# Optimization experiments

Hardware: AMD Instinct MI355X
Metric: run time of the kernel (lower is better)

Reference implementation:

```python
import jax, jax.numpy as jnp
import numpy as np

D_MODEL = 1024
N_HEADS = 16
D_HEAD = D_MODEL // N_HEADS
D_FF = 4096
B, T = 4, 2048
LN_EPS = 1e-5


def _layer_norm(x, gamma, beta):
    mu = jnp.mean(x, axis=-1, keepdims=True)
    var = jnp.var(x, axis=-1, keepdims=True)
    return (x - mu) * jax.lax.rsqrt(var + LN_EPS) * gamma + beta


def setup_inputs() -> dict:
    key = jax.random.key(0)
    ks = jax.random.split(key, 8)
    x = jax.random.normal(ks[0], (B, T, D_MODEL), dtype=jnp.float32)
    # causal mask: True = blocked (upper triangle above diagonal)
    attn_mask = ~jnp.tril(jnp.ones((T, T), dtype=bool))
    # xavier-uniform linear weights stored as [in, out] (pytorch applies x @ W.T)
    def xavier(k, fan_in, fan_out):
        lim = float(np.sqrt(6.0 / (fan_in + fan_out)))
        return jax.random.uniform(k, (fan_in, fan_out), jnp.float32, -lim, lim)
    Wq = xavier(ks[1], D_MODEL, D_MODEL); bq = jnp.zeros((D_MODEL,), jnp.float32)
    Wk = xavier(ks[2], D_MODEL, D_MODEL); bk = jnp.zeros((D_MODEL,), jnp.float32)
    Wv = xavier(ks[3], D_MODEL, D_MODEL); bv = jnp.zeros((D_MODEL,), jnp.float32)
    Wo = xavier(ks[4], D_MODEL, D_MODEL); bo = jnp.zeros((D_MODEL,), jnp.float32)
    W1 = xavier(ks[5], D_MODEL, D_FF); b1 = jnp.zeros((D_FF,), jnp.float32)
    W2 = 0.02 * jax.random.normal(ks[6], (D_FF, D_MODEL), jnp.float32)  # normal std=0.02 per _init_weights
    b2 = jnp.zeros((D_MODEL,), jnp.float32)
    g1 = jnp.ones((D_MODEL,), jnp.float32); be1 = jnp.zeros((D_MODEL,), jnp.float32)
    g2 = jnp.ones((D_MODEL,), jnp.float32); be2 = jnp.zeros((D_MODEL,), jnp.float32)
    return {"x": x, "attn_mask": attn_mask,
            "Wq": Wq, "bq": bq, "Wk": Wk, "bk": bk, "Wv": Wv, "bv": bv,
            "Wo": Wo, "bo": bo, "W1": W1, "b1": b1, "W2": W2, "b2": b2,
            "g1": g1, "be1": be1, "g2": g2, "be2": be2}


def reference(x, attn_mask, Wq, bq, Wk, bk, Wv, bv, Wo, bo, W1, b1, W2, b2, g1, be1, g2, be2):
    Bd, Td, Dd = x.shape
    residual = x
    x_n = _layer_norm(x, g1, be1)
    # projections -> (B, H, T, Dh)
    q = (x_n @ Wq + bq).reshape(Bd, Td, N_HEADS, D_HEAD).transpose(0, 2, 1, 3)
    k = (x_n @ Wk + bk).reshape(Bd, Td, N_HEADS, D_HEAD).transpose(0, 2, 1, 3)
    v = (x_n @ Wv + bv).reshape(Bd, Td, N_HEADS, D_HEAD).transpose(0, 2, 1, 3)
    scale = 1.0 / jnp.sqrt(jnp.asarray(D_HEAD, x.dtype))
    scores = jnp.einsum('bhqd,bhkd->bhqk', q, k) * scale  # (B,H,T,T)
    scores = jnp.where(attn_mask[None, None], -jnp.inf, scores)
    attn = jax.nn.softmax(scores, axis=-1)
    attn_out = jnp.einsum('bhqk,bhkd->bhqd', attn, v)
    attn_out = attn_out.transpose(0, 2, 1, 3).reshape(Bd, Td, Dd)
    attn_out = attn_out @ Wo + bo
    x = residual + attn_out  # dropout = identity (p=0 / eval)
    h = _layer_norm(x, g2, be2)
    h = jax.nn.gelu(h @ W1 + b1, approximate=False) @ W2 + b2
    return x + h
```

## Files before the change

kernel.cpp:

```cpp
#include <hip/hip_runtime.h>
#include <hip/hip_bf16.h>
#include <math.h>

#define TT   2048
#define DD   1024
#define HHD  16
#define FFD  4096
#define NTOK 8192

typedef __attribute__((ext_vector_type(8))) short bf16x8;
typedef __attribute__((ext_vector_type(4))) float f32x4;
typedef unsigned int u32;
#define AS(n) __attribute__((address_space(n)))

__device__ __forceinline__ unsigned short f2bf(float f) {
    u32 u = __builtin_bit_cast(u32, f);
    u += 0x7fffu + ((u >> 16) & 1u);
    return (unsigned short)(u >> 16);
}

__device__ __forceinline__ void gld_lds16(const void* g, void* l) {
    __builtin_amdgcn_global_load_lds((const AS(1) u32*)g, (AS(3) u32*)l, 16, 0, 0);
}

__device__ __forceinline__ int swz(int row) { return (row + (row >> 3)) & 7; }

__global__ __launch_bounds__(256) void wtrans(const float* __restrict__ W,
                                              unsigned short* __restrict__ Wt,
                                              int K, int N) {
    __shared__ float t[32][33];
    int tx = threadIdx.x & 31, ty = threadIdx.x >> 5;
    int n0 = blockIdx.x * 32, k0 = blockIdx.y * 32;
    #pragma unroll
    for (int i = 0; i < 32; i += 8)
        t[ty + i][tx] = W[(size_t)(k0 + ty + i) * N + n0 + tx];
    __syncthreads();
    #pragma unroll
    for (int i = 0; i < 32; i += 8)
        Wt[(size_t)(n0 + ty + i) * K + k0 + tx] = f2bf(t[tx][ty + i]);
}

__global__ __launch_bounds__(256) void ln_bf16(const float* __restrict__ x,
                                               const float* __restrict__ g,
                                               const float* __restrict__ be,
                                               unsigned short* __restrict__ y) {
    int tok = blockIdx.x, tid = threadIdx.x;
    float4 v = ((const float4*)(x + (size_t)tok * DD))[tid];
    float s  = v.x + v.y + v.z + v.w;
    float ss = v.x*v.x + v.y*v.y + v.z*v.z + v.w*v.w;
    #pragma unroll
    for (int m = 32; m >= 1; m >>= 1) { s += __shfl_xor(s, m); ss += __shfl_xor(ss, m); }
    __shared__ float red[8];
    if ((tid & 63) == 0) { red[tid >> 6] = s; red[4 + (tid >> 6)] = ss; }
    __syncthreads();
    s  = red[0] + red[1] + red[2] + red[3];
    ss = red[4] + red[5] + red[6] + red[7];
    float mu   = s * (1.0f / DD);
    float rstd = rsqrtf(ss * (1.0f / DD) - mu * mu + 1e-5f);
    float4 gv = ((const float4*)g)[tid];
    float4 bv = ((const float4*)be)[tid];
    ushort4 o;
    o.x = f2bf((v.x - mu) * rstd * gv.x + bv.x);
    o.y = f2bf((v.y - mu) * rstd * gv.y + bv.y);
    o.z = f2bf((v.z - mu) * rstd * gv.z + bv.z);
    o.w = f2bf((v.w - mu) * rstd * gv.w + bv.w);
    *(ushort4*)(y + (size_t)tok * DD + tid * 4) = o;
}

template <int MODE>
__global__ __launch_bounds__(256, 3) void gemm_bf16(const unsigned short* __restrict__ A,
                                                    const unsigned short* __restrict__ Bt,
                                                    const float* __restrict__ bias,
                                                    void* __restrict__ C,
                                                    const float* __restrict__ resid,
                                                    int M, int N, int K) {
    __shared__ __align__(16) unsigned short As[128 * 64];
    __shared__ __align__(16) unsigned short Bs[128 * 64];
    int tid = threadIdx.x, lane = tid & 63, w = tid >> 6;
    int wm = w >> 1, wn = w & 1;
    int m0 = blockIdx.y * 128, n0 = blockIdx.x * 128;
    int c = lane & 15, g = lane >> 4;

    f32x4 acc[4][4];
    f32x4 z4 = {0.f, 0.f, 0.f, 0.f};
    #pragma unroll
    for (int i = 0; i < 4; ++i)
        #pragma unroll
        for (int j = 0; j < 4; ++j) acc[i][j] = z4;

    const unsigned short* aSrc[4];
    const unsigned short* bSrc[4];
    int ldsOff[4];
    #pragma unroll
    for (int i = 0; i < 4; ++i) {
        int inst = w * 4 + i;
        int row  = inst * 8 + (lane >> 3);
        int kk   = ((lane & 7) ^ swz(row)) << 3;
        aSrc[i] = A  + (size_t)(m0 + row) * K + kk;
        bSrc[i] = Bt + (size_t)(n0 + row) * K + kk;
        ldsOff[i] = inst * 1024;
    }

    for (int k0 = 0; k0 < K; k0 += 64) {
        #pragma unroll
        for (int i = 0; i < 4; ++i) {
            gld_lds16(aSrc[i] + k0, (char*)As + ldsOff[i]);
            gld_lds16(bSrc[i] + k0, (char*)Bs + ldsOff[i]);
        }
        __syncthreads();
        #pragma unroll
        for (int ks = 0; ks < 2; ++ks) {
            bf16x8 af[4], bfr[4];
            int slot = ks * 4 + g;
            #pragma unroll
            for (int f = 0; f < 4; ++f) {
                int ra = wm * 64 + f * 16 + c;
                af[f]  = *(const bf16x8*)((const char*)As + ra * 128 + ((slot ^ swz(ra)) << 4));
                int rb = wn * 64 + f * 16 + c;
                bfr[f] = *(const bf16x8*)((const char*)Bs + rb * 128 + ((slot ^ swz(rb)) << 4));
            }
            #pragma unroll
            for (int i = 0; i < 4; ++i)
                #pragma unroll
                for (int j = 0; j < 4; ++j)
                    acc[i][j] = __builtin_amdgcn_mfma_f32_16x16x32_bf16(af[i], bfr[j], acc[i][j], 0, 0, 0);
        }
        __syncthreads();
    }

    float bcol[4];
    float4 brow[4];
    if (MODE == 4) {
        #pragma unroll
        for (int i = 0; i < 4; ++i)
            brow[i] = *(const float4*)&bias[m0 + wm * 64 + i * 16 + g * 4];
    } else {
        #pragma unroll
        for (int j = 0; j < 4; ++j) bcol[j] = bias[n0 + wn * 64 + j * 16 + c];
    }
    #pragma unroll
    for (int i = 0; i < 4; ++i) {
        #pragma unroll
        for (int r = 0; r < 4; ++r) {
            int rowm = m0 + wm * 64 + i * 16 + g * 4 + r;
            float br = (MODE == 4) ? ((const float*)&brow[i])[r] : 0.0f;
            #pragma unroll
            for (int j = 0; j < 4; ++j) {
                float val = acc[i][j][r] + ((MODE == 4) ? br : bcol[j]);
                int col = n0 + wn * 64 + j * 16 + c;
                if (MODE == 1) {
                    int b = rowm >> 11, t = rowm & 2047, h = col >> 6, d = col & 63;
                    ((unsigned short*)C)[(((size_t)((b << 4) + h) * TT + t) << 6) + d] = f2bf(val);
                } else if (MODE == 2) {
                    size_t idx = (size_t)rowm * N + col;
                    ((float*)C)[idx] = val + resid[idx];
                } else if (MODE == 3) {
                    float ge = 0.5f * val * (1.0f + erff(val * 0.70710678118f));
                    ((unsigned short*)C)[(size_t)rowm * N + col] = f2bf(ge);
                } else {
                    int b = col >> 11, t = col & 2047, h = rowm >> 6, d = rowm & 63;
                    ((unsigned short*)C)[(((size_t)((b << 4) + h) * 64 + d) << 11) + t] = f2bf(val);
                }
            }
        }
    }
}

__global__ __launch_bounds__(256, 4) void attn_bf16(const unsigned short* __restrict__ q,
                                                    const unsigned short* __restrict__ k,
                                                    const unsigned short* __restrict__ vt,
                                                    unsigned short* __restrict__ ao) {
    __shared__ __align__(16) unsigned short Ks[2][64 * 64];
    __shared__ __align__(16) unsigned short Vts[2][64 * 64];
    __shared__ __align__(16) unsigned short Ps[4][16 * 64];
    int tid = threadIdx.x, lane = tid & 63, w = tid >> 6;
    int bid = blockIdx.x;
    int bh  = (bid & 7) * 8 + ((bid >> 3) & 7);
    int pr  = bid >> 6;
    int c = lane & 15, g = lane >> 4;
    size_t kbase = (size_t)bh * TT * 64;
    size_t vbase = (size_t)bh * 64 * TT;

    const unsigned short* kSrc[2];
    const unsigned short* vSrc[2];
    int ldsOff[2];
    #pragma unroll
    for (int i = 0; i < 2; ++i) {
        int inst = w * 2 + i;
        int row  = inst * 8 + (lane >> 3);
        int kk   = ((lane & 7) ^ swz(row)) << 3;
        kSrc[i] = k  + kbase + (size_t)row * 64 + kk;
        vSrc[i] = vt + vbase + (size_t)row * TT + kk;
        ldsOff[i] = inst * 1024;
    }

    auto STAGE = [&](int buf, int kv0) {
        #pragma unroll
        for (int i = 0; i < 2; ++i) {
            gld_lds16(kSrc[i] + (size_t)kv0 * 64, (char*)Ks[buf] + ldsOff[i]);
            gld_lds16(vSrc[i] + kv0,              (char*)Vts[buf] + ldsOff[i]);
        }
    };

    int b = bh >> 4, h = bh & 15;
    f32x4 z4 = {0.f, 0.f, 0.f, 0.f};

    for (int ph = 0; ph < 2; ++ph) {
        int qt = ph ? (31 - pr) : pr;
        int q0 = qt * 64;
        int qrow = q0 + w * 16 + c;
        bf16x8 qf[2];
        qf[0] = *(const bf16x8*)(q + kbase + (size_t)qrow * 64 + g * 8);
        qf[1] = *(const bf16x8*)(q + kbase + (size_t)qrow * 64 + 32 + g * 8);

        float m_i[4], l_i[4];
        f32x4 o[4];
        #pragma unroll
        for (int j = 0; j < 4; ++j) { m_i[j] = -INFINITY; l_i[j] = 0.0f; o[j] = z4; }

        __syncthreads();
        STAGE(0, 0);

        for (int kt = 0; kt <= qt; ++kt) {
            int cur = kt & 1, kv0 = kt * 64;
            __syncthreads();
            if (kt < qt) STAGE(cur ^ 1, kv0 + 64);

            f32x4 s[4];
            #pragma unroll
            for (int f = 0; f < 4; ++f) s[f] = z4;
            __builtin_amdgcn_s_setprio(1);
            #pragma unroll
            for (int ks = 0; ks < 2; ++ks) {
                int slot = ks * 4 + g;
                #pragma unroll
                for (int f = 0; f < 4; ++f) {
                    int rb = f * 16 + c;
                    bf16x8 kf = *(const bf16x8*)((const char*)Ks[cur] + rb * 128 + ((slot ^ swz(rb)) << 4));
                    s[f] = __builtin_amdgcn_mfma_f32_16x16x32_bf16(qf[ks], kf, s[f], 0, 0, 0);
                }
            }
            __builtin_amdgcn_s_setprio(0);

            bool diag = (kt == qt);
            #pragma unroll
            for (int j = 0; j < 4; ++j) {
                int lq = g * 4 + j;
                int gq = q0 + w * 16 + lq;
                #pragma unroll
                for (int f = 0; f < 4; ++f) {
                    float sv = s[f][j] * 0.125f;
                    if (diag && (kv0 + f * 16 + c > gq)) sv = -INFINITY;
                    s[f][j] = sv;
                }
                float mx = fmaxf(fmaxf(s[0][j], s[1][j]), fmaxf(s[2][j], s[3][j]));
                #pragma unroll
                for (int mm = 8; mm >= 1; mm >>= 1) mx = fmaxf(mx, __shfl_xor(mx, mm));
                float newm = fmaxf(m_i[j], mx);
                float al = __expf(m_i[j] - newm);
                float rs = 0.0f;
                #pragma unroll
                for (int f = 0; f < 4; ++f) {
                    float p = __expf(s[f][j] - newm);
                    s[f][j] = p;
                    rs += p;
                }
                #pragma unroll
                for (int mm = 8; mm >= 1; mm >>= 1) rs += __shfl_xor(rs, mm);
                l_i[j] = l_i[j] * al + rs;
                m_i[j] = newm;
                #pragma unroll
                for (int f = 0; f < 4; ++f) {
                    int col = f * 16 + c;
                    int byte = lq * 128 + (((col >> 3) ^ swz(lq)) << 4) + ((col & 7) << 1);
                    *(unsigned short*)((char*)Ps[w] + byte) = f2bf(s[f][j]);
                }
                #pragma unroll
                for (int fd = 0; fd < 4; ++fd) o[fd][j] *= al;
            }
            asm volatile("s_waitcnt lgkmcnt(0)" ::: "memory");
            __builtin_amdgcn_sched_barrier(0);

            __builtin_amdgcn_s_setprio(1);
            #pragma unroll
            for (int ks = 0; ks < 2; ++ks) {
                int slot = ks * 4 + g;
                bf16x8 pa = *(const bf16x8*)((const char*)Ps[w] + c * 128 + ((slot ^ swz(c)) << 4));
                #pragma unroll
                for (int fd = 0; fd < 4; ++fd) {
                    int rv = fd * 16 + c;
                    bf16x8 vf = *(const bf16x8*)((const char*)Vts[cur] + rv * 128 + ((slot ^ swz(rv)) << 4));
                    o[fd] = __builtin_amdgcn_mfma_f32_16x16x32_bf16(pa, vf, o[fd], 0, 0, 0);
                }
            }
            __builtin_amdgcn_s_setprio(0);
        }

        #pragma unroll
        for (int fd = 0; fd < 4; ++fd)
            #pragma unroll
            for (int j = 0; j < 4; ++j) {
                int t = q0 + w * 16 + g * 4 + j;
                float val = o[fd][j] / l_i[j];
                ao[(((size_t)(b * TT + t)) << 10) + (h << 6) + fd * 16 + c] = f2bf(val);
            }
    }
}

extern "C" void kernel_launch(void* const* d_in, const int* in_sizes, int n_in,
                              void* d_out, int out_size, void* d_ws, size_t ws_size,
                              hipStream_t stream) {
    const float* x   = (const float*)d_in[0];
    const float* Wq  = (const float*)d_in[2];
    const float* bq  = (const float*)d_in[3];
    const float* Wk  = (const float*)d_in[4];
    const float* bk  = (const float*)d_in[5];
    const float* Wv  = (const float*)d_in[6];
    const float* bv  = (const float*)d_in[7];
    const float* Wo  = (const float*)d_in[8];
    const float* bo  = (const float*)d_in[9];
    const float* W1  = (const float*)d_in[10];
    const float* b1  = (const float*)d_in[11];
    const float* W2  = (const float*)d_in[12];
    const float* b2  = (const float*)d_in[13];
    const float* g1  = (const float*)d_in[14];
    const float* be1 = (const float*)d_in[15];
    const float* g2  = (const float*)d_in[16];
    const float* be2 = (const float*)d_in[17];

    float* out = (float*)d_out;
    char* w = (char*)d_ws;
    const size_t MB = 1024 * 1024;
    unsigned short* xnb = (unsigned short*)(w);
    unsigned short* qb  = (unsigned short*)(w + 16 * MB);
    unsigned short* kb  = (unsigned short*)(w + 32 * MB);
    unsigned short* vb  = (unsigned short*)(w + 48 * MB);
    unsigned short* aob = (unsigned short*)(w + 64 * MB);
    unsigned short* wqt = (unsigned short*)(w + 80 * MB);
    unsigned short* wkt = wqt + 1 * MB;
    unsigned short* wvt = wqt + 2 * MB;
    unsigned short* wot = wqt + 3 * MB;
    unsigned short* w1t = wqt + 4 * MB;
    unsigned short* w2t = w1t + 4 * MB;
    unsigned short* h1  = qb;

    dim3 blk(256);
    wtrans<<<dim3(DD / 32, DD / 32), blk, 0, stream>>>(Wq, wqt, DD, DD);
    wtrans<<<dim3(DD / 32, DD / 32), blk, 0, stream>>>(Wk, wkt, DD, DD);
    wtrans<<<dim3(DD / 32, DD / 32), blk, 0, stream>>>(Wv, wvt, DD, DD);
    wtrans<<<dim3(DD / 32, DD / 32), blk, 0, stream>>>(Wo, wot, DD, DD);
    wtrans<<<dim3(FFD / 32, DD / 32), blk, 0, stream>>>(W1, w1t, DD, FFD);
    wtrans<<<dim3(DD / 32, FFD / 32), blk, 0, stream>>>(W2, w2t, FFD, DD);

    ln_bf16<<<NTOK, blk, 0, stream>>>(x, g1, be1, xnb);

    dim3 gD(DD / 128, NTOK / 128);
    dim3 gF(FFD / 128, NTOK / 128);
    dim3 gV(NTOK / 128, DD / 128);
    gemm_bf16<1><<<gD, blk, 0, stream>>>(xnb, wqt, bq, qb, nullptr, NTOK, DD, DD);
    gemm_bf16<1><<<gD, blk, 0, stream>>>(xnb, wkt, bk, kb, nullptr, NTOK, DD, DD);
    gemm_bf16<4><<<gV, blk, 0, stream>>>(wvt, xnb, bv, vb, nullptr, DD, NTOK, DD);

    attn_bf16<<<dim3(1024), blk, 0, stream>>>(qb, kb, vb, aob);

    gemm_bf16<2><<<gD, blk, 0, stream>>>(aob, wot, bo, out, x, NTOK, DD, DD);
    ln_bf16<<<NTOK, blk, 0, stream>>>(out, g2, be2, xnb);
    gemm_bf16<3><<<gF, blk, 0, stream>>>(xnb, w1t, b1, h1, nullptr, NTOK, FFD, DD);
    gemm_bf16<2><<<gD, blk, 0, stream>>>(h1, w2t, b2, out, out, NTOK, DD, FFD);
}
```

Measured before the change: 586.4 us.

## Double-buffer GEMM with 256x128 tiles, 8 waves, and fold softmax scale into Q

Replaces the 128x128 single-buffered GEMM with a 512-thread, 256x128-tile kernel. It double-buffers LDS and interleaves the next tile's global-to-LDS loads with MFMA phases, using explicit barriers and priority hints. The attention softmax scale times log2(e) is folded into the Q projection epilogue, so attention can use exp2f and skip the per-element multiply. The risks are the heavier LDS use (96KB per block), fewer blocks for the smaller grids, and the hand-written barrier scheme being correct.

```diff
diff --git a/kernel.cpp b/kernel.cpp
--- a/kernel.cpp
+++ b/kernel.cpp
@@ -68,17 +68,17 @@
 }
 
 template <int MODE>
-__global__ __launch_bounds__(256, 3) void gemm_bf16(const unsigned short* __restrict__ A,
-                                                    const unsigned short* __restrict__ Bt,
-                                                    const float* __restrict__ bias,
-                                                    void* __restrict__ C,
-                                                    const float* __restrict__ resid,
-                                                    int M, int N, int K) {
-    __shared__ __align__(16) unsigned short As[128 * 64];
-    __shared__ __align__(16) unsigned short Bs[128 * 64];
+__global__ __launch_bounds__(512, 2) void gemm8(const unsigned short* __restrict__ A,
+                                                const unsigned short* __restrict__ Bt,
+                                                const float* __restrict__ bias,
+                                                void* __restrict__ C,
+                                                const float* __restrict__ resid,
+                                                float oscale, int M, int N, int K) {
+    __shared__ __align__(16) unsigned short As[2][256 * 64];
+    __shared__ __align__(16) unsigned short Bs[2][128 * 64];
     int tid = threadIdx.x, lane = tid & 63, w = tid >> 6;
     int wm = w >> 1, wn = w & 1;
-    int m0 = blockIdx.y * 128, n0 = blockIdx.x * 128;
+    int m0 = blockIdx.y * 256, n0 = blockIdx.x * 128;
     int c = lane & 15, g = lane >> 4;
 
     f32x4 acc[4][4];
@@ -88,44 +88,109 @@
         #pragma unroll
         for (int j = 0; j < 4; ++j) acc[i][j] = z4;
 
-    const unsigned short* aSrc[4];
-    const unsigned short* bSrc[4];
-    int ldsOff[4];
+    const unsigned short* aSrc[4]; int aOff[4];
+    const unsigned short* bSrc[2]; int bOff[2];
     #pragma unroll
     for (int i = 0; i < 4; ++i) {
         int inst = w * 4 + i;
         int row  = inst * 8 + (lane >> 3);
         int kk   = ((lane & 7) ^ swz(row)) << 3;
-        aSrc[i] = A  + (size_t)(m0 + row) * K + kk;
-        bSrc[i] = Bt + (size_t)(n0 + row) * K + kk;
-        ldsOff[i] = inst * 1024;
-    }
-
-    for (int k0 = 0; k0 < K; k0 += 64) {
-        #pragma unroll
-        for (int i = 0; i < 4; ++i) {
-            gld_lds16(aSrc[i] + k0, (char*)As + ldsOff[i]);
-            gld_lds16(bSrc[i] + k0, (char*)Bs + ldsOff[i]);
-        }
-        __syncthreads();
-        #pragma unroll
-        for (int ks = 0; ks < 2; ++ks) {
-            bf16x8 af[4], bfr[4];
-            int slot = ks * 4 + g;
-            #pragma unroll
-            for (int f = 0; f < 4; ++f) {
-                int ra = wm * 64 + f * 16 + c;
-                af[f]  = *(const bf16x8*)((const char*)As + ra * 128 + ((slot ^ swz(ra)) << 4));
-                int rb = wn * 64 + f * 16 + c;
-                bfr[f] = *(const bf16x8*)((const char*)Bs + rb * 128 + ((slot ^ swz(rb)) << 4));
-            }
-            #pragma unroll
-            for (int i = 0; i < 4; ++i)
-                #pragma unroll
-                for (int j = 0; j < 4; ++j)
-                    acc[i][j] = __builtin_amdgcn_mfma_f32_16x16x32_bf16(af[i], bfr[j], acc[i][j], 0, 0, 0);
-        }
-        __syncthreads();
+        aSrc[i] = A + (size_t)(m0 + row) * K + kk;
+        aOff[i] = inst * 1024;
+    }
+    #pragma unroll
+    for (int j = 0; j < 2; ++j) {
+        int inst = w * 2 + j;
+        int row  = inst * 8 + (lane >> 3);
+        int kk   = ((lane & 7) ^ swz(row)) << 3;
+        bSrc[j] = Bt + (size_t)(n0 + row) * K + kk;
+        bOff[j] = inst * 1024;
+    }
+
+    #pragma unroll
+    for (int i = 0; i < 4; ++i) gld_lds16(aSrc[i], (char*)As[0] + aOff[i]);
+    #pragma unroll
+    for (int j = 0; j < 2; ++j) gld_lds16(bSrc[j], (char*)Bs[0] + bOff[j]);
+
+    int NK = K >> 6;
+    for (int kt = 0; kt < NK; ++kt) {
+        int cur = kt & 1, nxt = cur ^ 1;
+        bool pre = (kt + 1 < NK);
+        int k1 = (kt + 1) << 6;
+        const char* Ab = (const char*)As[cur];
+        const char* Bb = (const char*)Bs[cur];
+        char* An = (char*)As[nxt];
+        char* Bn = (char*)Bs[nxt];
+        bf16x8 br[4], a0, a1, a2, a3;
+
+        if (pre) {
+            gld_lds16(aSrc[0] + k1, An + aOff[0]);
+            gld_lds16(aSrc[1] + k1, An + aOff[1]);
+            asm volatile("s_waitcnt vmcnt(2)" ::: "memory");
+        } else {
+            asm volatile("s_waitcnt vmcnt(0)" ::: "memory");
+        }
+        __builtin_amdgcn_sched_barrier(0);
+        asm volatile("s_barrier" ::: "memory");
+        #pragma unroll
+        for (int f = 0; f < 4; ++f) {
+            int rb = wn * 64 + f * 16 + c;
+            br[f] = *(const bf16x8*)(Bb + rb * 128 + ((g ^ swz(rb)) << 4));
+        }
+        { int ra = wm * 64 + c;      a0 = *(const bf16x8*)(Ab + ra * 128 + ((g ^ swz(ra)) << 4)); }
+        { int ra = wm * 64 + 16 + c; a1 = *(const bf16x8*)(Ab + ra * 128 + ((g ^ swz(ra)) << 4)); }
+        asm volatile("s_barrier" ::: "memory");
+        __builtin_amdgcn_s_setprio(1);
+        #pragma unroll
+        for (int j = 0; j < 4; ++j) acc[0][j] = __builtin_amdgcn_mfma_f32_16x16x32_bf16(a0, br[j], acc[0][j], 0, 0, 0);
+        #pragma unroll
+        for (int j = 0; j < 4; ++j) acc[1][j] = __builtin_amdgcn_mfma_f32_16x16x32_bf16(a1, br[j], acc[1][j], 0, 0, 0);
+        __builtin_amdgcn_s_setprio(0);
+
+        if (pre) {
+            gld_lds16(aSrc[2] + k1, An + aOff[2]);
+            gld_lds16(aSrc[3] + k1, An + aOff[3]);
+        }
+        { int ra = wm * 64 + 32 + c; a2 = *(const bf16x8*)(Ab + ra * 128 + ((g ^ swz(ra)) << 4)); }
+        { int ra = wm * 64 + 48 + c; a3 = *(const bf16x8*)(Ab + ra * 128 + ((g ^ swz(ra)) << 4)); }
+        asm volatile("s_barrier" ::: "memory");
+        __builtin_amdgcn_s_setprio(1);
+        #pragma unroll
+        for (int j = 0; j < 4; ++j) acc[2][j] = __builtin_amdgcn_mfma_f32_16x16x32_bf16(a2, br[j], acc[2][j], 0, 0, 0);
+        #pragma unroll
+        for (int j = 0; j < 4; ++j) acc[3][j] = __builtin_amdgcn_mfma_f32_16x16x32_bf16(a3, br[j], acc[3][j], 0, 0, 0);
+        __builtin_amdgcn_s_setprio(0);
+
+        if (pre) {
+            gld_lds16(bSrc[0] + k1, Bn + bOff[0]);
+            gld_lds16(bSrc[1] + k1, Bn + bOff[1]);
+        }
+        #pragma unroll
+        for (int f = 0; f < 4; ++f) {
+            int rb = wn * 64 + f * 16 + c;
+            br[f] = *(const bf16x8*)(Bb + rb * 128 + (((4 + g) ^ swz(rb)) << 4));
+        }
+        { int ra = wm * 64 + c;      a0 = *(const bf16x8*)(Ab + ra * 128 + (((4 + g) ^ swz(ra)) << 4)); }
+        { int ra = wm * 64 + 16 + c; a1 = *(const bf16x8*)(Ab + ra * 128 + (((4 + g) ^ swz(ra)) << 4)); }
+        asm volatile("s_barrier" ::: "memory");
+        __builtin_amdgcn_s_setprio(1);
+        #pragma unroll
+        for (int j = 0; j < 4; ++j) acc[0][j] = __builtin_amdgcn_mfma_f32_16x16x32_bf16(a0, br[j], acc[0][j], 0, 0, 0);
+        #pragma unroll
+        for (int j = 0; j < 4; ++j) acc[1][j] = __builtin_amdgcn_mfma_f32_16x16x32_bf16(a1, br[j], acc[1][j], 0, 0, 0);
+        __builtin_amdgcn_s_setprio(0);
+
+        { int ra = wm * 64 + 32 + c; a2 = *(const bf16x8*)(Ab + ra * 128 + (((4 + g) ^ swz(ra)) << 4)); }
+        { int ra = wm * 64 + 48 + c; a3 = *(const bf16x8*)(Ab + ra * 128 + (((4 + g) ^ swz(ra)) << 4)); }
+        asm volatile("s_waitcnt lgkmcnt(0)" ::: "memory");
+        __builtin_amdgcn_sched_barrier(0);
+        asm volatile("s_barrier" ::: "memory");
+        __builtin_amdgcn_s_setprio(1);
+        #pragma unroll
+        for (int j = 0; j < 4; ++j) acc[2][j] = __builtin_amdgcn_mfma_f32_16x16x32_bf16(a2, br[j], acc[2][j], 0, 0, 0);
+        #pragma unroll
+        for (int j = 0; j < 4; ++j) acc[3][j] = __builtin_amdgcn_mfma_f32_16x16x32_bf16(a3, br[j], acc[3][j], 0, 0, 0);
+        __builtin_amdgcn_s_setprio(0);
     }
 
     float bcol[4];
@@ -143,12 +208,13 @@
         #pragma unroll
         for (int r = 0; r < 4; ++r) {
             int rowm = m0 + wm * 64 + i * 16 + g * 4 + r;
-            float br = (MODE == 4) ? ((const float*)&brow[i])[r] : 0.0f;
+            float br_ = (MODE == 4) ? ((const float*)&brow[i])[r] : 0.0f;
             #pragma unroll
             for (int j = 0; j < 4; ++j) {
-                float val = acc[i][j][r] + ((MODE == 4) ? br : bcol[j]);
+                float val = acc[i][j][r] + ((MODE == 4) ? br_ : bcol[j]);
                 int col = n0 + wn * 64 + j * 16 + c;
                 if (MODE == 1) {
+                    val *= oscale;
                     int b = rowm >> 11, t = rowm & 2047, h = col >> 6, d = col & 63;
                     ((unsigned short*)C)[(((size_t)((b << 4) + h) * TT + t) << 6) + d] = f2bf(val);
                 } else if (MODE == 2) {
@@ -247,21 +313,20 @@
             for (int j = 0; j < 4; ++j) {
                 int lq = g * 4 + j;
                 int gq = q0 + w * 16 + lq;
-                #pragma unroll
-                for (int f = 0; f < 4; ++f) {
-                    float sv = s[f][j] * 0.125f;
-                    if (diag && (kv0 + f * 16 + c > gq)) sv = -INFINITY;
-                    s[f][j] = sv;
+                if (diag) {
+                    #pragma unroll
+                    for (int f = 0; f < 4; ++f)
+                        if (kv0 + f * 16 + c > gq) s[f][j] = -INFINITY;
                 }
                 float mx = fmaxf(fmaxf(s[0][j], s[1][j]), fmaxf(s[2][j], s[3][j]));
                 #pragma unroll
                 for (int mm = 8; mm >= 1; mm >>= 1) mx = fmaxf(mx, __shfl_xor(mx, mm));
                 float newm = fmaxf(m_i[j], mx);
-                float al = __expf(m_i[j] - newm);
+                float al = exp2f(m_i[j] - newm);
                 float rs = 0.0f;
                 #pragma unroll
                 for (int f = 0; f < 4; ++f) {
-                    float p = __expf(s[f][j] - newm);
+                    float p = exp2f(s[f][j] - newm);
                     s[f][j] = p;
                     rs += p;
                 }
@@ -354,17 +419,19 @@
 
     ln_bf16<<<NTOK, blk, 0, stream>>>(x, g1, be1, xnb);
 
-    dim3 gD(DD / 128, NTOK / 128);
-    dim3 gF(FFD / 128, NTOK / 128);
-    dim3 gV(NTOK / 128, DD / 128);
-    gemm_bf16<1><<<gD, blk, 0, stream>>>(xnb, wqt, bq, qb, nullptr, NTOK, DD, DD);
-    gemm_bf16<1><<<gD, blk, 0, stream>>>(xnb, wkt, bk, kb, nullptr, NTOK, DD, DD);
-    gemm_bf16<4><<<gV, blk, 0, stream>>>(wvt, xnb, bv, vb, nullptr, DD, NTOK, DD);
+    dim3 blk8(512);
+    const float QSCALE = 0.18033688011112042f;
+    dim3 gD(DD / 128, NTOK / 256);
+    dim3 gF(FFD / 128, NTOK / 256);
+    dim3 gV(NTOK / 128, DD / 256);
+    gemm8<1><<<gD, blk8, 0, stream>>>(xnb, wqt, bq, qb, nullptr, QSCALE, NTOK, DD, DD);
+    gemm8<1><<<gD, blk8, 0, stream>>>(xnb, wkt, bk, kb, nullptr, 1.0f, NTOK, DD, DD);
+    gemm8<4><<<gV, blk8, 0, stream>>>(wvt, xnb, bv, vb, nullptr, 1.0f, DD, NTOK, DD);
 
     attn_bf16<<<dim3(1024), blk, 0, stream>>>(qb, kb, vb, aob);
 
-    gemm_bf16<2><<<gD, blk, 0, stream>>>(aob, wot, bo, out, x, NTOK, DD, DD);
+    gemm8<2><<<gD, blk8, 0, stream>>>(aob, wot, bo, out, x, 1.0f, NTOK, DD, DD);
     ln_bf16<<<NTOK, blk, 0, stream>>>(out, g2, be2, xnb);
-    gemm_bf16<3><<<gF, blk, 0, stream>>>(xnb, w1t, b1, h1, nullptr, NTOK, FFD, DD);
-    gemm_bf16<2><<<gD, blk, 0, stream>>>(h1, w2t, b2, out, out, NTOK, DD, FFD);
-}
+    gemm8<3><<<gF, blk8, 0, stream>>>(xnb, w1t, b1, h1, nullptr, 1.0f, NTOK, FFD, DD);
+    gemm8<2><<<gD, blk8, 0, stream>>>(h1, w2t, b2, out, out, 1.0f, NTOK, DD, FFD);
+}
```

Measured after the change: 763.0 us. +30.1%, slower.
